# Kernel optimization log

Hardware: AMD Instinct MI355X
Metric: run time of the kernel (lower is better)

Reference implementation:

```python
import jax, jax.numpy as jnp
import numpy as np

VAR0, VAR1 = 0.1, 0.2          # SSD encode variances
POS_T, NEG_T, NPR = 0.5, 0.4, 3  # pos/neg thresholds, negpos_ratio
BBOX_ALPHA, CONF_ALPHA = 1.5, 1.0


def point_form(b):
    # cxcywh -> x1y1x2y2
    return jnp.concatenate([b[..., :2] - b[..., 2:] / 2, b[..., :2] + b[..., 2:] / 2], -1)


def jaccard(a, b):
    # a:[n,4], b:[m,4] in xyxy -> IoU [n,m]
    tl = jnp.maximum(a[:, None, :2], b[None, :, :2])
    br = jnp.minimum(a[:, None, 2:], b[None, :, 2:])
    inter = jnp.prod(jnp.clip(br - tl, 0.0), -1)
    area_a = jnp.prod(a[:, 2:] - a[:, :2], -1)[:, None]
    area_b = jnp.prod(b[:, 2:] - b[:, :2], -1)[None, :]
    return inter / jnp.clip(area_a + area_b - inter, 1e-10)


def encode(matched, priors):
    # matched: xyxy GT per prior; priors: cxcywh
    g_c = ((matched[:, :2] + matched[:, 2:]) / 2 - priors[:, :2]) / (VAR0 * priors[:, 2:])
    g_wh = jnp.log(jnp.clip((matched[:, 2:] - matched[:, :2]) / priors[:, 2:], 1e-8)) / VAR1
    return jnp.concatenate([g_c, g_wh], -1)


def match_one(gt_box, gt_lab, priors):
    # gt_box:[G,4] xyxy, gt_lab:[G], priors:[P,4] cxcywh
    ov = jaccard(gt_box, point_form(priors))            # [G,P]
    bt_over = ov.max(0)                                  # best GT overlap per prior [P]
    bt_idx = ov.argmax(0)                                # [P]
    bp_idx = ov.argmax(1)                                # best prior per GT [G]
    G = gt_box.shape[0]
    bt_over = bt_over.at[bp_idx].set(2.0)                # force-match best priors
    bt_idx = bt_idx.at[bp_idx].set(jnp.arange(G))
    matched = gt_box[bt_idx]                             # [P,4]
    conf_t = gt_lab[bt_idx]
    conf_t = jnp.where(bt_over < POS_T, jnp.where(bt_over < NEG_T, 0, -1), conf_t)
    return encode(matched, priors), conf_t


def reference(loc_data, conf_data, priors, gt_bboxes, gt_labels):
    B, P, C = conf_data.shape
    loc_t, conf_t = jax.vmap(match_one)(gt_bboxes, gt_labels, priors)
    loc_t = jax.lax.stop_gradient(loc_t)                 # targets are detached in torch
    pos = conf_t > 0                                     # [B,P]
    num_pos = pos.sum(-1)                                # [B]
    dt = loc_data.dtype
    pos_w = pos.astype(dt) / jnp.clip(num_pos, 1).astype(dt)[:, None]

    # localization: per-image-normalized smooth L1 over positives
    d = loc_data - loc_t
    sl1 = jnp.where(jnp.abs(d) < 1.0, 0.5 * d * d, jnp.abs(d) - 0.5)
    loss_B = (pos_w[:, :, None] * sl1).sum() * BBOX_ALPHA

    # OHEM confidence loss: mine top negpos_ratio*num_pos hardest negatives per image
    loss_c = jax.nn.logsumexp(conf_data, -1) - conf_data[..., 0]
    loss_c = jnp.where(pos | (conf_t < 0), 0.0, jax.lax.stop_gradient(loss_c))
    rank = jnp.argsort(jnp.argsort(-loss_c, -1), -1)     # descending rank [B,P]
    num_neg = jnp.clip(NPR * num_pos, 0, P - 1)
    neg = (rank < num_neg[:, None]) & (conf_t == 0)
    keep = (pos | neg).astype(dt)
    logp = jax.nn.log_softmax(conf_data, -1)
    tgt = jnp.clip(conf_t, 0)
    ce = -jnp.take_along_axis(logp, tgt[..., None], -1)[..., 0]
    loss_C = (keep * ce).sum() * CONF_ALPHA

    return jnp.stack([loss_B, loss_C]) / B               # [2]: (loss_B, loss_C)


def setup_inputs() -> dict:
    key = jax.random.key(0)
    k = jax.random.split(key, 8)
    B, P, C, G = 16, 19248, 81, 16
    loc_data = jax.random.normal(k[0], (B, P, 4), jnp.float32)
    conf_data = jax.random.normal(k[1], (B, P, C), jnp.float32)
    pc = jax.random.uniform(k[2], (B, P, 2)) * 0.9 + 0.05
    pwh = jax.random.uniform(k[3], (B, P, 2)) * 0.25 + 0.05
    priors = jnp.concatenate([pc, pwh], -1).astype(jnp.float32)  # cxcywh
    gc = jax.random.uniform(k[4], (B, G, 2)) * 0.8 + 0.1
    gwh = jax.random.uniform(k[5], (B, G, 2)) * 0.3 + 0.05
    gt_bboxes = jnp.clip(point_form(jnp.concatenate([gc, gwh], -1)), 0.0, 1.0).astype(jnp.float32)
    gt_labels = jax.random.randint(k[6], (B, G), 1, C)
    return {"loc_data": loc_data, "conf_data": conf_data, "priors": priors,
            "gt_bboxes": gt_bboxes, "gt_labels": gt_labels}
```

## Files before the change

### kernel.cpp

```cpp
#include <hip/hip_runtime.h>
#include <math.h>

#define NB 16
#define NP 19248
#define NC 81
#define NG 16
#define NBLK 76

static __device__ __forceinline__ float smoothl1(float d) {
    float a = fabsf(d);
    return (a < 1.f) ? 0.5f * d * d : (a - 0.5f);
}

static __device__ __forceinline__ unsigned long long umax64(unsigned long long a, unsigned long long b) {
    return a > b ? a : b;
}

__global__ void k_init(unsigned int* w, float* out) {
    if (threadIdx.x < 512) w[threadIdx.x] = 0u;
    if (threadIdx.x < 2) out[threadIdx.x] = 0.f;
}

__global__ void k_match(const float* __restrict__ priors,
                        const float* __restrict__ gtb,
                        float* __restrict__ bt_over, int* __restrict__ bt_idx,
                        unsigned long long* __restrict__ bp_key) {
    const int b = blockIdx.y;
    const int p = blockIdx.x * 256 + threadIdx.x;
    const bool valid = p < NP;
    __shared__ float4 sgt[NG];
    __shared__ unsigned long long smax[NG];
    if (threadIdx.x < NG) {
        const float* g4 = gtb + (size_t)(b * NG + threadIdx.x) * 4;
        sgt[threadIdx.x] = make_float4(g4[0], g4[1], g4[2], g4[3]);
        smax[threadIdx.x] = 0ULL;
    }
    __syncthreads();
    float4 pr = make_float4(0.f, 0.f, 0.f, 0.f);
    if (valid) pr = *(const float4*)(priors + ((size_t)b * NP + p) * 4);
    float px1 = pr.x - pr.z * 0.5f, py1 = pr.y - pr.w * 0.5f;
    float px2 = pr.x + pr.z * 0.5f, py2 = pr.y + pr.w * 0.5f;
    float areaP = (px2 - px1) * (py2 - py1);
    float best = -1.f; int bi = 0;
    unsigned int pk = 0xFFFFFFFFu - (unsigned int)p;
    #pragma unroll
    for (int g = 0; g < NG; ++g) {
        float4 gb = sgt[g];
        float iw = fminf(gb.z, px2) - fmaxf(gb.x, px1);
        float ih = fminf(gb.w, py2) - fmaxf(gb.y, py1);
        float inter = fmaxf(iw, 0.f) * fmaxf(ih, 0.f);
        float areaG = (gb.z - gb.x) * (gb.w - gb.y);
        float ov = inter / fmaxf(areaG + areaP - inter, 1e-10f);
        if (ov > best) { best = ov; bi = g; }
        unsigned long long key = ((unsigned long long)__float_as_uint(ov) << 32) | pk;
        #pragma unroll
        for (int off = 32; off >= 1; off >>= 1)
            key = umax64(key, (unsigned long long)__shfl_xor((unsigned long long)key, off));
        if ((threadIdx.x & 63) == 0) atomicMax(&smax[g], key);
    }
    if (valid) {
        bt_over[(size_t)b * NP + p] = best;
        bt_idx[(size_t)b * NP + p] = bi;
    }
    __syncthreads();
    if (threadIdx.x < NG) atomicMax(&bp_key[b * NG + threadIdx.x], smax[threadIdx.x]);
}

__global__ void __launch_bounds__(256, 4) k_conf(
        const float* __restrict__ conf,
        const float* __restrict__ loc,
        const float* __restrict__ priors,
        const float* __restrict__ gtb,
        const int* __restrict__ gtl,
        const float* __restrict__ bt_over,
        const int* __restrict__ bt_idx,
        const unsigned long long* __restrict__ bp_key,
        float* __restrict__ mlc,
        int* __restrict__ pnp, float* __restrict__ psl, float* __restrict__ pce) {
    const int b = blockIdx.y;
    const int p = blockIdx.x * 256 + threadIdx.x;
    const bool valid = p < NP;
    const int pc = valid ? p : (NP - 1);
    const int bp = b * NP + pc;

    const long long p81 = (long long)bp * 81;
    const int off = (int)(p81 & 3);
    const float4* q = (const float4*)(conf + (p81 - off));
    float4 r[21];
    #pragma unroll
    for (int i = 0; i < 21; ++i) r[i] = q[i];

    const float over = bt_over[bp];
    int bi = bt_idx[bp];
    int ct;
    if (over < 0.4f) ct = 0;
    else if (over < 0.5f) ct = -1;
    else ct = gtl[b * NG + bi];
    #pragma unroll
    for (int g = NG - 1; g >= 0; --g) {
        unsigned int fp = 0xFFFFFFFFu - (unsigned int)(bp_key[b * NG + g] & 0xFFFFFFFFULL);
        if (fp == (unsigned int)p) { bi = g; ct = gtl[b * NG + g]; break; }
    }
    if (!valid) ct = 0;
    const int tgt = ct > 0 ? ct : 0;

    float s0 = 0.f, s1 = 0.f, s2 = 0.f, s3 = 0.f;
    #pragma unroll
    for (int i = 0; i < 21; ++i) {
        float4 v = r[i];
        if (i == 0) {
            if (off <= 0) s0 += __expf(v.x);
            if (off <= 1) s1 += __expf(v.y);
            if (off <= 2) s2 += __expf(v.z);
            s3 += __expf(v.w);
        } else if (i == 20) {
            s0 += __expf(v.x);
            if (off >= 1) s1 += __expf(v.y);
            if (off >= 2) s2 += __expf(v.z);
            if (off >= 3) s3 += __expf(v.w);
        } else {
            s0 += __expf(v.x); s1 += __expf(v.y);
            s2 += __expf(v.z); s3 += __expf(v.w);
        }
    }
    const float s = (s0 + s1) + (s2 + s3);
    const float c0 = (off == 0) ? r[0].x : (off == 1) ? r[0].y : (off == 2) ? r[0].z : r[0].w;
    const float lse = __logf(s);

    if (valid) mlc[bp] = (ct == 0) ? (lse - c0) : -1.0f;

    float vsl = 0.f, vce = 0.f; int vnp = 0;
    if (ct > 0) {
        const float ctg = conf[p81 + tgt];
        const float4 pr = *(const float4*)(priors + (size_t)bp * 4);
        const float* gb = gtb + (size_t)(b * NG + bi) * 4;
        float lt0 = ((gb[0] + gb[2]) * 0.5f - pr.x) / (0.1f * pr.z);
        float lt1 = ((gb[1] + gb[3]) * 0.5f - pr.y) / (0.1f * pr.w);
        float lt2 = logf(fmaxf((gb[2] - gb[0]) / pr.z, 1e-8f)) / 0.2f;
        float lt3 = logf(fmaxf((gb[3] - gb[1]) / pr.w, 1e-8f)) / 0.2f;
        const float4 l4 = *(const float4*)(loc + (size_t)bp * 4);
        vsl = smoothl1(l4.x - lt0) + smoothl1(l4.y - lt1) +
              smoothl1(l4.z - lt2) + smoothl1(l4.w - lt3);
        vce = lse - ctg;
        vnp = 1;
    }
    #pragma unroll
    for (int o = 32; o >= 1; o >>= 1) {
        vnp += __shfl_xor(vnp, o);
        vsl += __shfl_xor(vsl, o);
        vce += __shfl_xor(vce, o);
    }
    __shared__ int snp[4]; __shared__ float ssl[4], sce2[4];
    const int w = threadIdx.x >> 6;
    if ((threadIdx.x & 63) == 0) { snp[w] = vnp; ssl[w] = vsl; sce2[w] = vce; }
    __syncthreads();
    if (threadIdx.x == 0) {
        const int idx = b * NBLK + blockIdx.x;
        pnp[idx] = snp[0] + snp[1] + snp[2] + snp[3];
        psl[idx] = ssl[0] + ssl[1] + ssl[2] + ssl[3];
        pce[idx] = sce2[0] + sce2[1] + sce2[2] + sce2[3];
    }
}

__global__ void __launch_bounds__(1024) k_selneg(
        const float* __restrict__ mlc,
        const int* __restrict__ pnp,
        const float* __restrict__ psl,
        const float* __restrict__ pce,
        float* __restrict__ out) {
    const int b = blockIdx.x, tid = threadIdx.x;
    __shared__ unsigned int hist[4096];
    __shared__ unsigned long long list[1024];
    __shared__ unsigned int s_jstar, s_need, s_cnt;
    __shared__ unsigned long long s_thr;
    __shared__ unsigned int wtot[16], wsuf[16];
    __shared__ float wsum[16];
    __shared__ int s_np; __shared__ float s_sl, s_cp;

    if (tid < 64) {
        int np_ = 0; float sl_ = 0.f, cp_ = 0.f;
        for (int i = tid; i < NBLK; i += 64) {
            np_ += pnp[b * NBLK + i];
            sl_ += psl[b * NBLK + i];
            cp_ += pce[b * NBLK + i];
        }
        #pragma unroll
        for (int o = 32; o >= 1; o >>= 1) {
            np_ += __shfl_xor(np_, o);
            sl_ += __shfl_xor(sl_, o);
            cp_ += __shfl_xor(cp_, o);
        }
        if (tid == 0) { s_np = np_; s_sl = sl_; s_cp = cp_; }
    }
    if (tid == 0) { s_cnt = 0u; s_thr = ~0ULL; }
    __syncthreads();
    const int np = s_np;
    const unsigned int k = (unsigned int)min(3 * np, NP - 1);
    const float4* v4 = (const float4*)(mlc + (size_t)b * NP);

    if (k > 0) {
        for (int i = tid; i < 4096; i += 1024) hist[i] = 0u;
        __syncthreads();
        for (int i = tid; i < NP / 4; i += 1024) {
            float4 v = v4[i];
            if (v.x >= 0.f) atomicAdd(&hist[min((unsigned int)(v.x * 256.f), 4095u)], 1u);
            if (v.y >= 0.f) atomicAdd(&hist[min((unsigned int)(v.y * 256.f), 4095u)], 1u);
            if (v.z >= 0.f) atomicAdd(&hist[min((unsigned int)(v.z * 256.f), 4095u)], 1u);
            if (v.w >= 0.f) atomicAdd(&hist[min((unsigned int)(v.w * 256.f), 4095u)], 1u);
        }
        __syncthreads();
        unsigned int c0 = hist[tid * 4], c1 = hist[tid * 4 + 1],
                     c2 = hist[tid * 4 + 2], c3 = hist[tid * 4 + 3];
        unsigned int t2 = c2 + c3, t1 = c1 + t2, t0 = c0 + t1;
        unsigned int s = t0;
        const int lane = tid & 63, w = tid >> 6;
        #pragma unroll
        for (int o = 1; o < 64; o <<= 1) {
            unsigned int vv = __shfl_down(s, o);
            if (lane + o < 64) s += vv;
        }
        if (lane == 0) wtot[w] = s;
        __syncthreads();
        if (tid < 16) {
            unsigned int acc = 0;
            for (int j = tid + 1; j < 16; ++j) acc += wtot[j];
            wsuf[tid] = acc;
        }
        __syncthreads();
        const unsigned int base = wsuf[w] + (s - t0);
        unsigned int b0 = base + t0, b1 = base + t1, b2 = base + t2, b3 = base + c3;
        hist[tid * 4] = b0; hist[tid * 4 + 1] = b1;
        hist[tid * 4 + 2] = b2; hist[tid * 4 + 3] = b3;
        __syncthreads();
        const unsigned int total = hist[0];
        if (k >= total) {
            if (tid == 0) s_thr = 0ULL;
        } else {
            unsigned int n3 = (tid * 4 + 4 < 4096) ? hist[tid * 4 + 4] : 0u;
            if (b0 >= k && b1 < k) { s_jstar = tid * 4;     s_need = k - b1; }
            if (b1 >= k && b2 < k) { s_jstar = tid * 4 + 1; s_need = k - b2; }
            if (b2 >= k && b3 < k) { s_jstar = tid * 4 + 2; s_need = k - b3; }
            if (b3 >= k && n3 < k) { s_jstar = tid * 4 + 3; s_need = k - n3; }
            __syncthreads();
            const unsigned int jstar = s_jstar, need = s_need;
            for (int i = tid; i < NP / 4; i += 1024) {
                float4 v = v4[i];
                float vv[4] = {v.x, v.y, v.z, v.w};
                #pragma unroll
                for (int c = 0; c < 4; ++c) {
                    if (vv[c] >= 0.f &&
                        min((unsigned int)(vv[c] * 256.f), 4095u) == jstar) {
                        unsigned int pos = atomicAdd(&s_cnt, 1u);
                        if (pos < 1024u)
                            list[pos] = ((unsigned long long)__float_as_uint(vv[c]) << 32) |
                                        (unsigned long long)(0xFFFFFFFFu - (unsigned int)(4 * i + c));
                    }
                }
            }
            __syncthreads();
            const unsigned int cnt = s_cnt;
            if (cnt <= 1024u) {
                if (tid < (int)cnt) {
                    unsigned long long me = list[tid];
                    unsigned int rk = 0;
                    for (unsigned int j = 0; j < cnt; ++j) rk += (list[j] > me) ? 1u : 0u;
                    if (rk == need - 1) s_thr = me;
                }
            } else if (tid == 0) {
                s_thr = ((unsigned long long)__float_as_uint((float)jstar / 256.f)) << 32;
            }
        }
    }
    __syncthreads();
    const unsigned long long thr = s_thr;

    float sum = 0.f;
    for (int i = tid; i < NP / 4; i += 1024) {
        float4 v = v4[i];
        float vv[4] = {v.x, v.y, v.z, v.w};
        #pragma unroll
        for (int c = 0; c < 4; ++c) {
            if (vv[c] >= 0.f) {
                unsigned long long key = ((unsigned long long)__float_as_uint(vv[c]) << 32) |
                                         (unsigned long long)(0xFFFFFFFFu - (unsigned int)(4 * i + c));
                if (key >= thr) sum += vv[c];
            }
        }
    }
    #pragma unroll
    for (int o = 32; o >= 1; o >>= 1) sum += __shfl_xor(sum, o);
    if ((tid & 63) == 0) wsum[tid >> 6] = sum;
    __syncthreads();
    if (tid == 0) {
        float neg = 0.f;
        #pragma unroll
        for (int i = 0; i < 16; ++i) neg += wsum[i];
        float lb = s_sl / (float)max(np, 1);
        float lc = s_cp + neg;
        atomicAdd(&out[0], lb * 1.5f / (float)NB);
        atomicAdd(&out[1], lc / (float)NB);
    }
}

extern "C" void kernel_launch(void* const* d_in, const int* in_sizes, int n_in,
                              void* d_out, int out_size, void* d_ws, size_t ws_size,
                              hipStream_t stream) {
    const float* loc    = (const float*)d_in[0];
    const float* conf   = (const float*)d_in[1];
    const float* priors = (const float*)d_in[2];
    const float* gtb    = (const float*)d_in[3];
    const int*   gtl    = (const int*)d_in[4];
    float* out = (float*)d_out;

    char* w = (char*)d_ws;
    const size_t BP4 = (size_t)NB * NP * 4;
    unsigned long long* bp_key = (unsigned long long*)w;
    int*   pnp = (int*)  (w + 4096);
    float* psl = (float*)(w + 4096 + NB * NBLK * 4);
    float* pce = (float*)(w + 4096 + 2 * NB * NBLK * 4);
    float* bt_over  = (float*)(w + 32768);
    int*   bt_idx   = (int*)  (w + 32768 + BP4);
    float* mlc      = (float*)(w + 32768 + 2 * BP4);

    k_init<<<1, 512, 0, stream>>>((unsigned int*)w, out);
    k_match<<<dim3(NBLK, NB), 256, 0, stream>>>(priors, gtb, bt_over, bt_idx, bp_key);
    k_conf<<<dim3(NBLK, NB), 256, 0, stream>>>(conf, loc, priors, gtb, gtl,
                                               bt_over, bt_idx, bp_key, mlc,
                                               pnp, psl, pce);
    k_selneg<<<NB, 1024, 0, stream>>>(mlc, pnp, psl, pce, out);
}
```

Before: 189.4 us.

## Stage conf rows through LDS with 4 lanes per prior; register-cache mlc in selneg

k_conf now loads 16 contiguous conf rows per wave into shared memory with coalesced float4 copies, and each prior is handled by 4 lanes that split the softmax sum and gather the target logit. The grid grows to 301 blocks per image, giving more parallelism than one thread per prior with 21 strided float4 loads each. Partial sums are written per wave instead of per block. k_selneg loads its mlc row into registers once and reuses it for the histogram, candidate and sum passes instead of reading global memory three times. k_match also shortens its shuffle reduction to 16 lanes with more atomics. The extra shared memory and the 4-lane split add some redundant work per prior.

```diff
diff --git a/kernel.cpp b/kernel.cpp
--- a/kernel.cpp
+++ b/kernel.cpp
@@ -6,6 +6,8 @@
 #define NC 81
 #define NG 16
 #define NBLK 76
+#define NBC 301
+#define NWPB (NBC * 4)
 
 static __device__ __forceinline__ float smoothl1(float d) {
     float a = fabsf(d);
@@ -54,9 +56,9 @@
         if (ov > best) { best = ov; bi = g; }
         unsigned long long key = ((unsigned long long)__float_as_uint(ov) << 32) | pk;
         #pragma unroll
-        for (int off = 32; off >= 1; off >>= 1)
+        for (int off = 1; off <= 8; off <<= 1)
             key = umax64(key, (unsigned long long)__shfl_xor((unsigned long long)key, off));
-        if ((threadIdx.x & 63) == 0) atomicMax(&smax[g], key);
+        if ((threadIdx.x & 15) == 0) atomicMax(&smax[g], key);
     }
     if (valid) {
         bt_over[(size_t)b * NP + p] = best;
@@ -66,7 +68,7 @@
     if (threadIdx.x < NG) atomicMax(&bp_key[b * NG + threadIdx.x], smax[threadIdx.x]);
 }
 
-__global__ void __launch_bounds__(256, 4) k_conf(
+__global__ void __launch_bounds__(256, 6) k_conf(
         const float* __restrict__ conf,
         const float* __restrict__ loc,
         const float* __restrict__ priors,
@@ -77,18 +79,24 @@
         const unsigned long long* __restrict__ bp_key,
         float* __restrict__ mlc,
         int* __restrict__ pnp, float* __restrict__ psl, float* __restrict__ pce) {
+    __shared__ float sc[4][1296];
     const int b = blockIdx.y;
-    const int p = blockIdx.x * 256 + threadIdx.x;
-    const bool valid = p < NP;
-    const int pc = valid ? p : (NP - 1);
-    const int bp = b * NP + pc;
-
-    const long long p81 = (long long)bp * 81;
-    const int off = (int)(p81 & 3);
-    const float4* q = (const float4*)(conf + (p81 - off));
-    float4 r[21];
-    #pragma unroll
-    for (int i = 0; i < 21; ++i) r[i] = q[i];
+    const int tid = threadIdx.x;
+    const int w = tid >> 6, lane = tid & 63;
+    const int rb = blockIdx.x * 64 + w * 16;
+    const bool wvalid = rb < NP;
+    const int rb_c = wvalid ? rb : (NP - 16);
+
+    const float4* src = (const float4*)(conf + ((size_t)b * NP + rb_c) * 81);
+    float4* dst = (float4*)sc[w];
+    #pragma unroll
+    for (int i = 0; i < 5; ++i) dst[lane + 64 * i] = src[lane + 64 * i];
+    if (lane < 4) dst[lane + 320] = src[lane + 320];
+    __builtin_amdgcn_wave_barrier();
+
+    const int r = lane >> 2, c = lane & 3;
+    const int p = rb_c + r;
+    const int bp = b * NP + p;
 
     const float over = bt_over[bp];
     int bi = bt_idx[bp];
@@ -101,43 +109,35 @@
         unsigned int fp = 0xFFFFFFFFu - (unsigned int)(bp_key[b * NG + g] & 0xFFFFFFFFULL);
         if (fp == (unsigned int)p) { bi = g; ct = gtl[b * NG + g]; break; }
     }
-    if (!valid) ct = 0;
+    if (!wvalid) ct = 0;
     const int tgt = ct > 0 ? ct : 0;
 
-    float s0 = 0.f, s1 = 0.f, s2 = 0.f, s3 = 0.f;
-    #pragma unroll
-    for (int i = 0; i < 21; ++i) {
-        float4 v = r[i];
-        if (i == 0) {
-            if (off <= 0) s0 += __expf(v.x);
-            if (off <= 1) s1 += __expf(v.y);
-            if (off <= 2) s2 += __expf(v.z);
-            s3 += __expf(v.w);
-        } else if (i == 20) {
-            s0 += __expf(v.x);
-            if (off >= 1) s1 += __expf(v.y);
-            if (off >= 2) s2 += __expf(v.z);
-            if (off >= 3) s3 += __expf(v.w);
-        } else {
-            s0 += __expf(v.x); s1 += __expf(v.y);
-            s2 += __expf(v.z); s3 += __expf(v.w);
-        }
-    }
-    const float s = (s0 + s1) + (s2 + s3);
-    const float c0 = (off == 0) ? r[0].x : (off == 1) ? r[0].y : (off == 2) ? r[0].z : r[0].w;
+    const float* row = sc[w] + r * 81;
+    float s = 0.f, ctg = 0.f;
+    #pragma unroll
+    for (int k = 0; k < 21; ++k) {
+        int cc = c + 4 * k;
+        if (cc < 81) {
+            float v = row[cc];
+            s += __expf(v);
+            ctg += (cc == tgt) ? v : 0.f;
+        }
+    }
+    s += __shfl_xor(s, 1, 4);   s += __shfl_xor(s, 2, 4);
+    ctg += __shfl_xor(ctg, 1, 4); ctg += __shfl_xor(ctg, 2, 4);
+    const float c0 = row[0];
     const float lse = __logf(s);
 
-    if (valid) mlc[bp] = (ct == 0) ? (lse - c0) : -1.0f;
+    if (c == 0 && wvalid) mlc[bp] = (ct == 0) ? (lse - c0) : -1.0f;
 
     float vsl = 0.f, vce = 0.f; int vnp = 0;
-    if (ct > 0) {
-        const float ctg = conf[p81 + tgt];
-        const float4 pr = *(const float4*)(priors + (size_t)bp * 4);
+    if (c == 0 && ct > 0) {
+        const float4 prr = *(const float4*)(priors + (size_t)bp * 4);
         const float* gb = gtb + (size_t)(b * NG + bi) * 4;
-        float lt0 = ((gb[0] + gb[2]) * 0.5f - pr.x) / (0.1f * pr.z);
-        float lt1 = ((gb[1] + gb[3]) * 0.5f - pr.y) / (0.1f * pr.w);
-        float lt2 = logf(fmaxf((gb[2] - gb[0]) / pr.z, 1e-8f)) / 0.2f;
-        float lt3 = logf(fmaxf((gb[3] - gb[1]) / pr.w, 1e-8f)) / 0.2f;
+        float lt0 = ((gb[0] + gb[2]) * 0.5f - prr.x) / (0.1f * prr.z);
+        float lt1 = ((gb[1] + gb[3]) * 0.5f - prr.y) / (0.1f * prr.w);
+        float lt2 = logf(fmaxf((gb[2] - gb[0]) / prr.z, 1e-8f)) / 0.2f;
+        float lt3 = logf(fmaxf((gb[3] - gb[1]) / prr.w, 1e-8f)) / 0.2f;
         const float4 l4 = *(const float4*)(loc + (size_t)bp * 4);
         vsl = smoothl1(l4.x - lt0) + smoothl1(l4.y - lt1) +
               smoothl1(l4.z - lt2) + smoothl1(l4.w - lt3);
@@ -150,15 +150,9 @@
         vsl += __shfl_xor(vsl, o);
         vce += __shfl_xor(vce, o);
     }
-    __shared__ int snp[4]; __shared__ float ssl[4], sce2[4];
-    const int w = threadIdx.x >> 6;
-    if ((threadIdx.x & 63) == 0) { snp[w] = vnp; ssl[w] = vsl; sce2[w] = vce; }
-    __syncthreads();
-    if (threadIdx.x == 0) {
-        const int idx = b * NBLK + blockIdx.x;
-        pnp[idx] = snp[0] + snp[1] + snp[2] + snp[3];
-        psl[idx] = ssl[0] + ssl[1] + ssl[2] + ssl[3];
-        pce[idx] = sce2[0] + sce2[1] + sce2[2] + sce2[3];
+    if (lane == 0) {
+        const int idx = b * NWPB + blockIdx.x * 4 + w;
+        pnp[idx] = vnp; psl[idx] = vsl; pce[idx] = vce;
     }
 }
 
@@ -175,14 +169,23 @@
     __shared__ unsigned long long s_thr;
     __shared__ unsigned int wtot[16], wsuf[16];
     __shared__ float wsum[16];
+    __shared__ int wnp[16]; __shared__ float wsl[16], wcp[16];
     __shared__ int s_np; __shared__ float s_sl, s_cp;
 
-    if (tid < 64) {
+    const float4* v4 = (const float4*)(mlc + (size_t)b * NP);
+    float4 rv[5];
+    #pragma unroll
+    for (int j = 0; j < 5; ++j) {
+        int i = tid + 1024 * j;
+        rv[j] = (i < NP / 4) ? v4[i] : make_float4(-1.f, -1.f, -1.f, -1.f);
+    }
+
+    {
         int np_ = 0; float sl_ = 0.f, cp_ = 0.f;
-        for (int i = tid; i < NBLK; i += 64) {
-            np_ += pnp[b * NBLK + i];
-            sl_ += psl[b * NBLK + i];
-            cp_ += pce[b * NBLK + i];
+        for (int i = tid; i < NWPB; i += 1024) {
+            np_ += pnp[b * NWPB + i];
+            sl_ += psl[b * NWPB + i];
+            cp_ += pce[b * NWPB + i];
         }
         #pragma unroll
         for (int o = 32; o >= 1; o >>= 1) {
@@ -190,25 +193,30 @@
             sl_ += __shfl_xor(sl_, o);
             cp_ += __shfl_xor(cp_, o);
         }
-        if (tid == 0) { s_np = np_; s_sl = sl_; s_cp = cp_; }
+        if ((tid & 63) == 0) { wnp[tid >> 6] = np_; wsl[tid >> 6] = sl_; wcp[tid >> 6] = cp_; }
     }
     if (tid == 0) { s_cnt = 0u; s_thr = ~0ULL; }
+    for (int i = tid; i < 4096; i += 1024) hist[i] = 0u;
+    __syncthreads();
+    if (tid == 0) {
+        int np_ = 0; float sl_ = 0.f, cp_ = 0.f;
+        #pragma unroll
+        for (int i = 0; i < 16; ++i) { np_ += wnp[i]; sl_ += wsl[i]; cp_ += wcp[i]; }
+        s_np = np_; s_sl = sl_; s_cp = cp_;
+    }
+    #pragma unroll
+    for (int j = 0; j < 5; ++j) {
+        float vv[4] = {rv[j].x, rv[j].y, rv[j].z, rv[j].w};
+        #pragma unroll
+        for (int c = 0; c < 4; ++c)
+            if (vv[c] >= 0.f)
+                atomicAdd(&hist[min((unsigned int)(vv[c] * 256.f), 4095u)], 1u);
+    }
     __syncthreads();
     const int np = s_np;
     const unsigned int k = (unsigned int)min(3 * np, NP - 1);
-    const float4* v4 = (const float4*)(mlc + (size_t)b * NP);
 
     if (k > 0) {
-        for (int i = tid; i < 4096; i += 1024) hist[i] = 0u;
-        __syncthreads();
-        for (int i = tid; i < NP / 4; i += 1024) {
-            float4 v = v4[i];
-            if (v.x >= 0.f) atomicAdd(&hist[min((unsigned int)(v.x * 256.f), 4095u)], 1u);
-            if (v.y >= 0.f) atomicAdd(&hist[min((unsigned int)(v.y * 256.f), 4095u)], 1u);
-            if (v.z >= 0.f) atomicAdd(&hist[min((unsigned int)(v.z * 256.f), 4095u)], 1u);
-            if (v.w >= 0.f) atomicAdd(&hist[min((unsigned int)(v.w * 256.f), 4095u)], 1u);
-        }
-        __syncthreads();
         unsigned int c0 = hist[tid * 4], c1 = hist[tid * 4 + 1],
                      c2 = hist[tid * 4 + 2], c3 = hist[tid * 4 + 3];
         unsigned int t2 = c2 + c3, t1 = c1 + t2, t0 = c0 + t1;
@@ -243,17 +251,19 @@
             if (b3 >= k && n3 < k) { s_jstar = tid * 4 + 3; s_need = k - n3; }
             __syncthreads();
             const unsigned int jstar = s_jstar, need = s_need;
-            for (int i = tid; i < NP / 4; i += 1024) {
-                float4 v = v4[i];
-                float vv[4] = {v.x, v.y, v.z, v.w};
+            #pragma unroll
+            for (int j = 0; j < 5; ++j) {
+                float vv[4] = {rv[j].x, rv[j].y, rv[j].z, rv[j].w};
                 #pragma unroll
                 for (int c = 0; c < 4; ++c) {
                     if (vv[c] >= 0.f &&
                         min((unsigned int)(vv[c] * 256.f), 4095u) == jstar) {
                         unsigned int pos = atomicAdd(&s_cnt, 1u);
-                        if (pos < 1024u)
+                        if (pos < 1024u) {
+                            int pidx = 4 * (tid + 1024 * j) + c;
                             list[pos] = ((unsigned long long)__float_as_uint(vv[c]) << 32) |
-                                        (unsigned long long)(0xFFFFFFFFu - (unsigned int)(4 * i + c));
+                                        (unsigned long long)(0xFFFFFFFFu - (unsigned int)pidx);
+                        }
                     }
                 }
             }
@@ -275,14 +285,15 @@
     const unsigned long long thr = s_thr;
 
     float sum = 0.f;
-    for (int i = tid; i < NP / 4; i += 1024) {
-        float4 v = v4[i];
-        float vv[4] = {v.x, v.y, v.z, v.w};
+    #pragma unroll
+    for (int j = 0; j < 5; ++j) {
+        float vv[4] = {rv[j].x, rv[j].y, rv[j].z, rv[j].w};
         #pragma unroll
         for (int c = 0; c < 4; ++c) {
             if (vv[c] >= 0.f) {
+                int pidx = 4 * (tid + 1024 * j) + c;
                 unsigned long long key = ((unsigned long long)__float_as_uint(vv[c]) << 32) |
-                                         (unsigned long long)(0xFFFFFFFFu - (unsigned int)(4 * i + c));
+                                         (unsigned long long)(0xFFFFFFFFu - (unsigned int)pidx);
                 if (key >= thr) sum += vv[c];
             }
         }
@@ -314,18 +325,19 @@
 
     char* w = (char*)d_ws;
     const size_t BP4 = (size_t)NB * NP * 4;
+    const size_t P1  = (size_t)NB * NWPB * 4;
     unsigned long long* bp_key = (unsigned long long*)w;
     int*   pnp = (int*)  (w + 4096);
-    float* psl = (float*)(w + 4096 + NB * NBLK * 4);
-    float* pce = (float*)(w + 4096 + 2 * NB * NBLK * 4);
-    float* bt_over  = (float*)(w + 32768);
-    int*   bt_idx   = (int*)  (w + 32768 + BP4);
-    float* mlc      = (float*)(w + 32768 + 2 * BP4);
+    float* psl = (float*)(w + 4096 + P1);
+    float* pce = (float*)(w + 4096 + 2 * P1);
+    float* bt_over  = (float*)(w + 262144);
+    int*   bt_idx   = (int*)  (w + 262144 + BP4);
+    float* mlc      = (float*)(w + 262144 + 2 * BP4);
 
     k_init<<<1, 512, 0, stream>>>((unsigned int*)w, out);
     k_match<<<dim3(NBLK, NB), 256, 0, stream>>>(priors, gtb, bt_over, bt_idx, bp_key);
-    k_conf<<<dim3(NBLK, NB), 256, 0, stream>>>(conf, loc, priors, gtb, gtl,
-                                               bt_over, bt_idx, bp_key, mlc,
-                                               pnp, psl, pce);
+    k_conf<<<dim3(NBC, NB), 256, 0, stream>>>(conf, loc, priors, gtb, gtl,
+                                              bt_over, bt_idx, bp_key, mlc,
+                                              pnp, psl, pce);
     k_selneg<<<NB, 1024, 0, stream>>>(mlc, pnp, psl, pce, out);
 }
```

Result: no change. 188.0 us (-0.7%).
